# Performance work log

Measured on AMD Instinct MI355X. Metric: run time of the kernel, lower is better.

## Reference

```python
import jax, jax.numpy as jnp
import numpy as np

D_MODEL = 1024
NUM_LATENTS = 8
N_HEADS = 8
HEAD_DIM = D_MODEL // N_HEADS
LN_EPS = 1e-5
NEG_INF = -1e9


def setup_inputs() -> dict:
    key = jax.random.key(0)
    ks = jax.random.split(key, 9)
    B, S, d = 8, 8192, D_MODEL
    hidden_states = jax.random.normal(ks[0], (B, S, d), dtype=jnp.float32)
    attention_mask = jax.random.randint(ks[1], (B, S), 0, 2, dtype=jnp.int32)
    # guarantee at least one valid token per row
    attention_mask = attention_mask.at[:, 0].set(1)
    latent_queries = jax.random.normal(ks[2], (NUM_LATENTS, d), dtype=jnp.float32) * 0.02
    lim = 1.0 / np.sqrt(d)
    in_proj_weight = jax.random.uniform(ks[3], (3 * d, d), minval=-lim, maxval=lim, dtype=jnp.float32)
    in_proj_bias = jnp.zeros((3 * d,), jnp.float32)
    out_proj_weight = jax.random.uniform(ks[4], (d, d), minval=-lim, maxval=lim, dtype=jnp.float32)
    out_proj_bias = jnp.zeros((d,), jnp.float32)
    ln_gamma = jnp.ones((d,), jnp.float32)
    ln_beta = jnp.zeros((d,), jnp.float32)
    return {
        "hidden_states": hidden_states,
        "latent_queries": latent_queries,
        "in_proj_weight": in_proj_weight,
        "in_proj_bias": in_proj_bias,
        "out_proj_weight": out_proj_weight,
        "out_proj_bias": out_proj_bias,
        "ln_gamma": ln_gamma,
        "ln_beta": ln_beta,
        "attention_mask": attention_mask,
    }


def reference(hidden_states, latent_queries, in_proj_weight, in_proj_bias,
              out_proj_weight, out_proj_bias, ln_gamma, ln_beta, attention_mask):
    B, S, d = hidden_states.shape
    K, H, hd = NUM_LATENTS, N_HEADS, HEAD_DIM
    Wq, Wk, Wv = jnp.split(in_proj_weight, 3, axis=0)   # each [d, d]
    bq, bk, bv = jnp.split(in_proj_bias, 3, axis=0)
    # projections (queries shared over batch)
    q = latent_queries @ Wq.T + bq                      # [K, d]
    k = hidden_states @ Wk.T + bk                       # [B, S, d]
    v = hidden_states @ Wv.T + bv                       # [B, S, d]
    q = q.reshape(K, H, hd).transpose(1, 0, 2)          # [H, K, hd]
    k = k.reshape(B, S, H, hd).transpose(0, 2, 1, 3)    # [B, H, S, hd]
    v = v.reshape(B, S, H, hd).transpose(0, 2, 1, 3)    # [B, H, S, hd]
    scale = 1.0 / np.sqrt(hd)
    scores = jnp.einsum('hkd,bhsd->bhks', q, k) * scale  # [B, H, K, S]
    pad = (attention_mask == 0)[:, None, None, :]        # [B, 1, 1, S]
    scores = jnp.where(pad, NEG_INF, scores)
    attn = jax.nn.softmax(scores, axis=-1)
    ctx = jnp.einsum('bhks,bhsd->bhkd', attn, v)         # [B, H, K, hd]
    ctx = ctx.transpose(0, 2, 1, 3).reshape(B, K, d)     # [B, K, d]
    pooled = ctx @ out_proj_weight.T + out_proj_bias     # [B, K, d]
    # LayerNorm
    mu = pooled.mean(-1, keepdims=True)
    var = jnp.mean(jnp.square(pooled - mu), axis=-1, keepdims=True)
    pooled = (pooled - mu) * jax.lax.rsqrt(var + LN_EPS) * ln_gamma + ln_beta
    return pooled.mean(axis=1)                           # [B, d]
```

## Files before the change

kernel.cpp:

```cpp
#include <hip/hip_runtime.h>
#include <math.h>

#define D_M 1024
#define S_L 8192
#define B_N 8
#define H_N 8
#define HD_ 128
#define HK_ 64
#define SCALE_ 0.08838834764831845f
#define NEG_INF_ -1e9f
#define PITCH_ 40
#define AP_ 72

typedef _Float16 half8v __attribute__((ext_vector_type(8)));
typedef _Float16 half4v __attribute__((ext_vector_type(4)));
typedef float floatx4 __attribute__((ext_vector_type(4)));

__global__ void k_q(const float* __restrict__ lat, const float* __restrict__ W,
                    const float* __restrict__ bias, float* __restrict__ q) {
  int g = blockIdx.x * blockDim.x + threadIdx.x;
  int kidx = g >> 10, i = g & 1023;
  const float* wr = W + (size_t)i * D_M;
  const float* lr = lat + kidx * D_M;
  float acc = bias[i];
  #pragma unroll 4
  for (int t = 0; t < D_M; t += 4) {
    float4 w = *(const float4*)(wr + t);
    float4 l = *(const float4*)(lr + t);
    acc += w.x*l.x + w.y*l.y + w.z*l.z + w.w*l.w;
  }
  q[g] = acc;
}

__global__ void k_qt(const float* __restrict__ q, const float* __restrict__ W,
                     const float* __restrict__ bias, _Float16* __restrict__ qth,
                     float* __restrict__ qconst) {
  int g = blockIdx.x * blockDim.x + threadIdx.x;
  int hk = g >> 10, j = g & 1023;
  int h = hk >> 3, kidx = hk & 7;
  const float* qr = q + kidx * D_M + h * HD_;
  const float* wb = W + ((size_t)D_M + (size_t)h * HD_) * D_M + j;
  float acc = 0.f;
  #pragma unroll 4
  for (int dd = 0; dd < HD_; ++dd)
    acc += qr[dd] * wb[(size_t)dd * D_M];
  qth[g] = (_Float16)(acc * SCALE_);
  if (j == 0) {
    const float* bk = bias + D_M + h * HD_;
    float c = 0.f;
    for (int dd = 0; dd < HD_; ++dd) c += qr[dd] * bk[dd];
    qconst[hk] = c * SCALE_;
  }
}

__global__ __launch_bounds__(256) void k_scores3(
    const float* __restrict__ hsrc, const _Float16* __restrict__ qth,
    const float* __restrict__ qc, const int* __restrict__ mask,
    _Float16* __restrict__ ph, float* __restrict__ pm, float* __restrict__ pl) {
  __shared__ __align__(16) _Float16 As[128 * AP_];
  __shared__ __align__(16) _Float16 Bs[64 * AP_];
  __shared__ _Float16 pT[128][68];
  __shared__ int smask[128];
  __shared__ float qcs[64];
  const int tid = threadIdx.x;
  const int b = blockIdx.x >> 6;
  const int st = blockIdx.x & 63;
  const int s0 = st * 128;
  const int w = tid >> 6, l = tid & 63;
  const int row16 = l & 15, kc = l >> 4;
  if (tid < 128) smask[tid] = mask[b * S_L + s0 + tid];
  if (tid < 64) qcs[tid] = qc[tid];
  floatx4 acc[2][4];
  #pragma unroll
  for (int mf = 0; mf < 2; ++mf)
    #pragma unroll
    for (int nf = 0; nf < 4; ++nf) acc[mf][nf] = (floatx4){0.f, 0.f, 0.f, 0.f};

  const int r_ = tid >> 3, c_ = tid & 7;
  const float* hb = hsrc + ((size_t)b * S_L + s0) * D_M;
  float4 fa[4][2];
  half8v fb[2];
  #pragma unroll
  for (int p = 0; p < 4; ++p) {
    const float* pr = hb + (size_t)(p * 32 + r_) * D_M + c_ * 8;
    fa[p][0] = *(const float4*)pr; fa[p][1] = *(const float4*)(pr + 4);
  }
  fb[0] = *(const half8v*)(qth + (size_t)r_ * D_M + c_ * 8);
  fb[1] = *(const half8v*)(qth + (size_t)(r_ + 32) * D_M + c_ * 8);

  for (int k0 = 0; k0 < D_M; k0 += 64) {
    __syncthreads();
    #pragma unroll
    for (int p = 0; p < 4; ++p) {
      half8v hv;
      hv[0] = (_Float16)fa[p][0].x; hv[1] = (_Float16)fa[p][0].y;
      hv[2] = (_Float16)fa[p][0].z; hv[3] = (_Float16)fa[p][0].w;
      hv[4] = (_Float16)fa[p][1].x; hv[5] = (_Float16)fa[p][1].y;
      hv[6] = (_Float16)fa[p][1].z; hv[7] = (_Float16)fa[p][1].w;
      *(half8v*)&As[(p * 32 + r_) * AP_ + c_ * 8] = hv;
    }
    *(half8v*)&Bs[r_ * AP_ + c_ * 8] = fb[0];
    *(half8v*)&Bs[(r_ + 32) * AP_ + c_ * 8] = fb[1];
    if (k0 + 64 < D_M) {
      #pragma unroll
      for (int p = 0; p < 4; ++p) {
        const float* pr = hb + (size_t)(p * 32 + r_) * D_M + (k0 + 64) + c_ * 8;
        fa[p][0] = *(const float4*)pr; fa[p][1] = *(const float4*)(pr + 4);
      }
      fb[0] = *(const half8v*)(qth + (size_t)r_ * D_M + (k0 + 64) + c_ * 8);
      fb[1] = *(const half8v*)(qth + (size_t)(r_ + 32) * D_M + (k0 + 64) + c_ * 8);
    }
    __syncthreads();
    #pragma unroll
    for (int kk = 0; kk < 2; ++kk) {
      half8v af[2], bf4[4];
      #pragma unroll
      for (int mf = 0; mf < 2; ++mf)
        af[mf] = *(const half8v*)&As[(w * 32 + mf * 16 + row16) * AP_ + kk * 32 + kc * 8];
      #pragma unroll
      for (int nf = 0; nf < 4; ++nf)
        bf4[nf] = *(const half8v*)&Bs[(nf * 16 + row16) * AP_ + kk * 32 + kc * 8];
      #pragma unroll
      for (int mf = 0; mf < 2; ++mf)
        #pragma unroll
        for (int nf = 0; nf < 4; ++nf)
          acc[mf][nf] = __builtin_amdgcn_mfma_f32_16x16x32_f16(af[mf], bf4[nf], acc[mf][nf], 0, 0, 0);
    }
  }
  int msk[8];
  #pragma unroll
  for (int mf = 0; mf < 2; ++mf)
    #pragma unroll
    for (int r = 0; r < 4; ++r)
      msk[mf * 4 + r] = smask[w * 32 + mf * 16 + kc * 4 + r];
  #pragma unroll
  for (int nf = 0; nf < 4; ++nf) {
    int hk = nf * 16 + row16;
    float qcv = qcs[hk];
    float vals[8];
    float mloc = -3.4e38f;
    #pragma unroll
    for (int mf = 0; mf < 2; ++mf)
      #pragma unroll
      for (int r = 0; r < 4; ++r) {
        float v = msk[mf * 4 + r] ? (acc[mf][nf][r] + qcv) : NEG_INF_;
        vals[mf * 4 + r] = v;
        mloc = fmaxf(mloc, v);
      }
    mloc = fmaxf(mloc, __shfl_xor(mloc, 16, 64));
    mloc = fmaxf(mloc, __shfl_xor(mloc, 32, 64));
    float ls = 0.f;
    #pragma unroll
    for (int mf = 0; mf < 2; ++mf)
      #pragma unroll
      for (int r = 0; r < 4; ++r) {
        float e = __expf(vals[mf * 4 + r] - mloc);
        ls += e;
        pT[w * 32 + mf * 16 + kc * 4 + r][hk] = (_Float16)e;
      }
    ls += __shfl_xor(ls, 16, 64);
    ls += __shfl_xor(ls, 32, 64);
    if (kc == 0) {
      int idx = ((b * 64 + st) * 4 + w) * 64 + hk;
      pm[idx] = mloc;
      pl[idx] = ls;
    }
  }
  __syncthreads();
  {
    int hk2 = tid >> 2, q4 = tid & 3;
    _Float16* dst = ph + ((size_t)b * 64 + hk2) * S_L + s0 + q4 * 32;
    #pragma unroll
    for (int i = 0; i < 4; ++i) {
      half8v v;
      #pragma unroll
      for (int e = 0; e < 8; ++e) v[e] = pT[q4 * 32 + i * 8 + e][hk2];
      *(half8v*)(dst + i * 8) = v;
    }
  }
}

__global__ __launch_bounds__(256) void k_stats2b(
    const float* __restrict__ pm, const float* __restrict__ pl,
    float* __restrict__ lvinv, _Float16* __restrict__ ph) {
  __shared__ float red[256];
  int bh = blockIdx.x;
  int b = bh >> 6, hk = bh & 63;
  int tid = threadIdx.x;
  float m = pm[((size_t)b * 256 + tid) * 64 + hk];
  float lv = pl[((size_t)b * 256 + tid) * 64 + hk];
  red[tid] = m; __syncthreads();
  for (int off = 128; off > 0; off >>= 1) {
    if (tid < off) red[tid] = fmaxf(red[tid], red[tid + off]);
    __syncthreads();
  }
  float M = red[0]; __syncthreads();
  red[tid] = lv * __expf(m - M); __syncthreads();
  for (int off = 128; off > 0; off >>= 1) {
    if (tid < off) red[tid] += red[tid + off];
    __syncthreads();
  }
  if (tid == 0) lvinv[bh] = 1.f / red[0];
  float f = __expf(m - M);
  _Float16* pp = ph + (size_t)bh * S_L + tid * 32;
  #pragma unroll
  for (int i = 0; i < 4; ++i) {
    half8v v = *(half8v*)(pp + i * 8);
    #pragma unroll
    for (int e = 0; e < 8; ++e) v[e] = (_Float16)((float)v[e] * f);
    *(half8v*)(pp + i * 8) = v;
  }
}

__global__ __launch_bounds__(512) void k_part(
    const float* __restrict__ hsrc, const _Float16* __restrict__ ph,
    float* __restrict__ part) {
  __shared__ __align__(16) _Float16 htile[512 * PITCH_];
  const int tid = threadIdx.x;
  const int b  = blockIdx.x >> 5;
  const int jb = (blockIdx.x >> 4) & 1;
  const int sc = blockIdx.x & 15;
  const int w = tid >> 6, l = tid & 63;
  const int row16 = l & 15, kc = l >> 4;
  const int s_base = sc * 512;
  const float* hb = hsrc + (size_t)b * S_L * D_M + jb * 512;
  const _Float16* phb = ph + (size_t)b * HK_ * S_L;
  floatx4 acc[4][4];
  #pragma unroll
  for (int mf = 0; mf < 4; ++mf)
    #pragma unroll
    for (int nf = 0; nf < 4; ++nf) acc[mf][nf] = (floatx4){0.f, 0.f, 0.f, 0.f};

  const int jcol = tid;
  float colv[32];
  #pragma unroll
  for (int s = 0; s < 32; ++s)
    colv[s] = hb[(size_t)(s_base + s) * D_M + jcol];

  for (int t = 0; t < 16; ++t) {
    const int s0 = s_base + t * 32;
    __syncthreads();
    #pragma unroll
    for (int sb = 0; sb < 8; ++sb) {
      half4v hv;
      hv[0] = (_Float16)colv[sb * 4 + 0];
      hv[1] = (_Float16)colv[sb * 4 + 1];
      hv[2] = (_Float16)colv[sb * 4 + 2];
      hv[3] = (_Float16)colv[sb * 4 + 3];
      *(half4v*)&htile[jcol * PITCH_ + sb * 4] = hv;
    }
    __syncthreads();
    if (t < 15) {
      #pragma unroll
      for (int s = 0; s < 32; ++s)
        colv[s] = hb[(size_t)(s0 + 32 + s) * D_M + jcol];
    }
    half8v ap[4];
    #pragma unroll
    for (int mf = 0; mf < 4; ++mf)
      ap[mf] = *(const half8v*)(phb + (size_t)(mf * 16 + row16) * S_L + s0 + kc * 8);
    #pragma unroll
    for (int nf = 0; nf < 4; ++nf) {
      int j = w * 64 + nf * 16 + row16;
      half8v bv = *(const half8v*)&htile[j * PITCH_ + kc * 8];
      #pragma unroll
      for (int mf = 0; mf < 4; ++mf)
        acc[mf][nf] = __builtin_amdgcn_mfma_f32_16x16x32_f16(ap[mf], bv, acc[mf][nf], 0, 0, 0);
    }
  }
  #pragma unroll
  for (int mf = 0; mf < 4; ++mf)
    #pragma unroll
    for (int nf = 0; nf < 4; ++nf) {
      int j = w * 64 + nf * 16 + row16;
      #pragma unroll
      for (int r = 0; r < 4; ++r) {
        int hk = mf * 16 + kc * 4 + r;
        part[(((size_t)(b * 2 + jb) * 16 + sc) * HK_ + hk) * 512 + j] = acc[mf][nf][r];
      }
    }
}

__global__ void k_comb(const float* __restrict__ part, const float* __restrict__ lvinv,
                       float* __restrict__ ctxh) {
  int g = blockIdx.x * blockDim.x + threadIdx.x;
  int b = g >> 14;
  int rem = g & 16383;
  int hk = rem >> 8;
  int j4 = rem & 255;
  int jb = j4 >> 7;
  int jr4 = j4 & 127;
  const float* pb = part + ((size_t)(b * 2 + jb) * 16 * HK_ + hk) * 512 + jr4 * 4;
  float4 s = make_float4(0.f, 0.f, 0.f, 0.f);
  #pragma unroll
  for (int sc = 0; sc < 16; ++sc) {
    float4 v = *(const float4*)(pb + (size_t)sc * HK_ * 512);
    s.x += v.x; s.y += v.y; s.z += v.z; s.w += v.w;
  }
  float li = lvinv[b * 64 + hk];
  s.x *= li; s.y *= li; s.z *= li; s.w *= li;
  *(float4*)(ctxh + ((size_t)b * HK_ + hk) * D_M + j4 * 4) = s;
}

__global__ void k_ctx(const float* __restrict__ ctxh, const float* __restrict__ W,
                      const float* __restrict__ bias, float* __restrict__ ctx) {
  int g2 = blockIdx.x * blockDim.x + threadIdx.x;
  int o = g2 >> 2, kq = g2 & 3;
  int b = o >> 13, kidx = (o >> 10) & 7, i = o & 1023;
  int hk = (i >> 7) * 8 + kidx;
  const float* wr = W + ((size_t)2 * D_M + i) * D_M + kq * 256;
  const float* xr = ctxh + ((size_t)b * HK_ + hk) * D_M + kq * 256;
  float acc = 0.f;
  #pragma unroll 8
  for (int t = 0; t < 256; t += 4) {
    float4 w = *(const float4*)(wr + t);
    float4 x = *(const float4*)(xr + t);
    acc += w.x*x.x + w.y*x.y + w.z*x.z + w.w*x.w;
  }
  acc += __shfl_xor(acc, 1, 64);
  acc += __shfl_xor(acc, 2, 64);
  if (kq == 0) ctx[o] = acc + bias[2 * D_M + i];
}

__global__ void k_pool(const float* __restrict__ ctx, const float* __restrict__ W,
                       const float* __restrict__ bias, float* __restrict__ pooled) {
  int g2 = blockIdx.x * blockDim.x + threadIdx.x;
  int o = g2 >> 2, kq = g2 & 3;
  int b = o >> 13, kidx = (o >> 10) & 7, i = o & 1023;
  const float* wr = W + (size_t)i * D_M + kq * 256;
  const float* xr = ctx + ((size_t)b * 8 + kidx) * D_M + kq * 256;
  float acc = 0.f;
  #pragma unroll 8
  for (int t = 0; t < 256; t += 4) {
    float4 w = *(const float4*)(wr + t);
    float4 x = *(const float4*)(xr + t);
    acc += w.x*x.x + w.y*x.y + w.z*x.z + w.w*x.w;
  }
  acc += __shfl_xor(acc, 1, 64);
  acc += __shfl_xor(acc, 2, 64);
  if (kq == 0) pooled[o] = acc + bias[i];
}

__global__ void k_ln(const float* __restrict__ pooled, const float* __restrict__ gamma,
                     const float* __restrict__ beta, float* __restrict__ out) {
  __shared__ float red[256];
  int b = blockIdx.x, tid = threadIdx.x;
  float acc[4] = {0.f, 0.f, 0.f, 0.f};
  for (int kidx = 0; kidx < 8; ++kidx) {
    const float* row = pooled + ((size_t)b * 8 + kidx) * D_M;
    float v[4]; float s = 0.f;
    #pragma unroll
    for (int c = 0; c < 4; ++c) { v[c] = row[tid + 256 * c]; s += v[c]; }
    red[tid] = s; __syncthreads();
    for (int off = 128; off > 0; off >>= 1) {
      if (tid < off) red[tid] += red[tid + off];
      __syncthreads();
    }
    float mu = red[0] * (1.f / 1024.f);
    __syncthreads();
    float ss = 0.f;
    #pragma unroll
    for (int c = 0; c < 4; ++c) { float dd = v[c] - mu; ss += dd * dd; }
    red[tid] = ss; __syncthreads();
    for (int off = 128; off > 0; off >>= 1) {
      if (tid < off) red[tid] += red[tid + off];
      __syncthreads();
    }
    float rstd = rsqrtf(red[0] * (1.f / 1024.f) + 1e-5f);
    __syncthreads();
    #pragma unroll
    for (int c = 0; c < 4; ++c) {
      int i = tid + 256 * c;
      acc[c] += ((v[c] - mu) * rstd * gamma[i] + beta[i]) * 0.125f;
    }
  }
  #pragma unroll
  for (int c = 0; c < 4; ++c) out[(size_t)b * D_M + tid + 256 * c] = acc[c];
}

extern "C" void kernel_launch(void* const* d_in, const int* in_sizes, int n_in,
                              void* d_out, int out_size, void* d_ws, size_t ws_size,
                              hipStream_t stream) {
  const float* hidden = (const float*)d_in[0];
  const float* latent = (const float*)d_in[1];
  const float* w_in   = (const float*)d_in[2];
  const float* b_in   = (const float*)d_in[3];
  const float* w_out  = (const float*)d_in[4];
  const float* b_out  = (const float*)d_in[5];
  const float* gamma  = (const float*)d_in[6];
  const float* beta   = (const float*)d_in[7];
  const int*   mask   = (const int*)d_in[8];
  float* out = (float*)d_out;
  float* ws = (float*)d_ws;
  float* q      = ws;
  float* qc     = q + 8192;
  float* lvinv  = qc + 64;
  float* pm     = lvinv + 512;
  float* pl     = pm + 131072;
  _Float16* qth = (_Float16*)(pl + 131072);
  _Float16* ph  = (_Float16*)(pl + 131072 + 32768);
  float* part   = pl + 131072 + 32768 + 2097152;
  float* ctxh   = part + 8388608;
  float* ctx    = ctxh + 524288;
  float* pooled = ctx + 65536;

  k_q       <<<32,   256, 0, stream>>>(latent, w_in, b_in, q);
  k_qt      <<<256,  256, 0, stream>>>(q, w_in, b_in, qth, qc);
  k_scores3 <<<512,  256, 0, stream>>>(hidden, qth, qc, mask, ph, pm, pl);
  k_stats2b <<<512,  256, 0, stream>>>(pm, pl, lvinv, ph);
  k_part    <<<256,  512, 0, stream>>>(hidden, ph, part);
  k_comb    <<<512,  256, 0, stream>>>(part, lvinv, ctxh);
  k_ctx     <<<1024, 256, 0, stream>>>(ctxh, w_in, b_in, ctx);
  k_pool    <<<1024, 256, 0, stream>>>(ctx, w_out, b_out, pooled);
  k_ln      <<<8,    256, 0, stream>>>(pooled, gamma, beta, out);
}
```

Before: 315.3 us.

## Defer softmax rescale into k_part and double thread parallelism in scores/part kernels

k_scores3 now runs 512 threads per block, each wave owning 16 rows instead of 32, and reuses the As buffer for the transposed probability tile to cut LDS. The stats kernel no longer rewrites the fp16 probability buffer. It emits per-tile scale factors instead, which k_part applies while loading the probabilities, removing a full read-modify-write pass over ph. k_part splits the column dimension into four blocks of 256, giving 512 blocks with fewer accumulators each. The cost is more sync overhead per unit of work, extra scale loads and multiplies in k_part, and re-reading the probability rows across four column blocks.

```diff
diff --git a/kernel.cpp b/kernel.cpp
--- a/kernel.cpp
+++ b/kernel.cpp
@@ -53,13 +53,12 @@
   }
 }
 
-__global__ __launch_bounds__(256) void k_scores3(
+__global__ __launch_bounds__(512, 2) void k_scores3(
     const float* __restrict__ hsrc, const _Float16* __restrict__ qth,
     const float* __restrict__ qc, const int* __restrict__ mask,
     _Float16* __restrict__ ph, float* __restrict__ pm, float* __restrict__ pl) {
   __shared__ __align__(16) _Float16 As[128 * AP_];
   __shared__ __align__(16) _Float16 Bs[64 * AP_];
-  __shared__ _Float16 pT[128][68];
   __shared__ int smask[128];
   __shared__ float qcs[64];
   const int tid = threadIdx.x;
@@ -70,198 +69,181 @@
   const int row16 = l & 15, kc = l >> 4;
   if (tid < 128) smask[tid] = mask[b * S_L + s0 + tid];
   if (tid < 64) qcs[tid] = qc[tid];
-  floatx4 acc[2][4];
-  #pragma unroll
-  for (int mf = 0; mf < 2; ++mf)
-    #pragma unroll
-    for (int nf = 0; nf < 4; ++nf) acc[mf][nf] = (floatx4){0.f, 0.f, 0.f, 0.f};
+  floatx4 acc[4];
+  #pragma unroll
+  for (int nf = 0; nf < 4; ++nf) acc[nf] = (floatx4){0.f, 0.f, 0.f, 0.f};
 
   const int r_ = tid >> 3, c_ = tid & 7;
   const float* hb = hsrc + ((size_t)b * S_L + s0) * D_M;
-  float4 fa[4][2];
-  half8v fb[2];
-  #pragma unroll
-  for (int p = 0; p < 4; ++p) {
-    const float* pr = hb + (size_t)(p * 32 + r_) * D_M + c_ * 8;
+  float4 fa[2][2];
+  half8v fb;
+  #pragma unroll
+  for (int p = 0; p < 2; ++p) {
+    const float* pr = hb + (size_t)(p * 64 + r_) * D_M + c_ * 8;
     fa[p][0] = *(const float4*)pr; fa[p][1] = *(const float4*)(pr + 4);
   }
-  fb[0] = *(const half8v*)(qth + (size_t)r_ * D_M + c_ * 8);
-  fb[1] = *(const half8v*)(qth + (size_t)(r_ + 32) * D_M + c_ * 8);
+  fb = *(const half8v*)(qth + (size_t)r_ * D_M + c_ * 8);
 
   for (int k0 = 0; k0 < D_M; k0 += 64) {
     __syncthreads();
     #pragma unroll
-    for (int p = 0; p < 4; ++p) {
+    for (int p = 0; p < 2; ++p) {
       half8v hv;
       hv[0] = (_Float16)fa[p][0].x; hv[1] = (_Float16)fa[p][0].y;
       hv[2] = (_Float16)fa[p][0].z; hv[3] = (_Float16)fa[p][0].w;
       hv[4] = (_Float16)fa[p][1].x; hv[5] = (_Float16)fa[p][1].y;
       hv[6] = (_Float16)fa[p][1].z; hv[7] = (_Float16)fa[p][1].w;
-      *(half8v*)&As[(p * 32 + r_) * AP_ + c_ * 8] = hv;
-    }
-    *(half8v*)&Bs[r_ * AP_ + c_ * 8] = fb[0];
-    *(half8v*)&Bs[(r_ + 32) * AP_ + c_ * 8] = fb[1];
+      *(half8v*)&As[(p * 64 + r_) * AP_ + c_ * 8] = hv;
+    }
+    *(half8v*)&Bs[r_ * AP_ + c_ * 8] = fb;
     if (k0 + 64 < D_M) {
       #pragma unroll
-      for (int p = 0; p < 4; ++p) {
-        const float* pr = hb + (size_t)(p * 32 + r_) * D_M + (k0 + 64) + c_ * 8;
+      for (int p = 0; p < 2; ++p) {
+        const float* pr = hb + (size_t)(p * 64 + r_) * D_M + (k0 + 64) + c_ * 8;
         fa[p][0] = *(const float4*)pr; fa[p][1] = *(const float4*)(pr + 4);
       }
-      fb[0] = *(const half8v*)(qth + (size_t)r_ * D_M + (k0 + 64) + c_ * 8);
-      fb[1] = *(const half8v*)(qth + (size_t)(r_ + 32) * D_M + (k0 + 64) + c_ * 8);
+      fb = *(const half8v*)(qth + (size_t)r_ * D_M + (k0 + 64) + c_ * 8);
     }
     __syncthreads();
     #pragma unroll
     for (int kk = 0; kk < 2; ++kk) {
-      half8v af[2], bf4[4];
-      #pragma unroll
-      for (int mf = 0; mf < 2; ++mf)
-        af[mf] = *(const half8v*)&As[(w * 32 + mf * 16 + row16) * AP_ + kk * 32 + kc * 8];
-      #pragma unroll
-      for (int nf = 0; nf < 4; ++nf)
-        bf4[nf] = *(const half8v*)&Bs[(nf * 16 + row16) * AP_ + kk * 32 + kc * 8];
-      #pragma unroll
-      for (int mf = 0; mf < 2; ++mf)
-        #pragma unroll
-        for (int nf = 0; nf < 4; ++nf)
-          acc[mf][nf] = __builtin_amdgcn_mfma_f32_16x16x32_f16(af[mf], bf4[nf], acc[mf][nf], 0, 0, 0);
-    }
-  }
-  int msk[8];
-  #pragma unroll
-  for (int mf = 0; mf < 2; ++mf)
-    #pragma unroll
-    for (int r = 0; r < 4; ++r)
-      msk[mf * 4 + r] = smask[w * 32 + mf * 16 + kc * 4 + r];
+      half8v af = *(const half8v*)&As[(w * 16 + row16) * AP_ + kk * 32 + kc * 8];
+      #pragma unroll
+      for (int nf = 0; nf < 4; ++nf) {
+        half8v bf = *(const half8v*)&Bs[(nf * 16 + row16) * AP_ + kk * 32 + kc * 8];
+        acc[nf] = __builtin_amdgcn_mfma_f32_16x16x32_f16(af, bf, acc[nf], 0, 0, 0);
+      }
+    }
+  }
+  __syncthreads();
+  _Float16 (*pT)[68] = (_Float16 (*)[68])As;
+  int msk[4];
+  #pragma unroll
+  for (int r = 0; r < 4; ++r) msk[r] = smask[w * 16 + kc * 4 + r];
   #pragma unroll
   for (int nf = 0; nf < 4; ++nf) {
     int hk = nf * 16 + row16;
     float qcv = qcs[hk];
-    float vals[8];
+    float vals[4];
     float mloc = -3.4e38f;
     #pragma unroll
-    for (int mf = 0; mf < 2; ++mf)
-      #pragma unroll
-      for (int r = 0; r < 4; ++r) {
-        float v = msk[mf * 4 + r] ? (acc[mf][nf][r] + qcv) : NEG_INF_;
-        vals[mf * 4 + r] = v;
-        mloc = fmaxf(mloc, v);
-      }
+    for (int r = 0; r < 4; ++r) {
+      float v = msk[r] ? (acc[nf][r] + qcv) : NEG_INF_;
+      vals[r] = v;
+      mloc = fmaxf(mloc, v);
+    }
     mloc = fmaxf(mloc, __shfl_xor(mloc, 16, 64));
     mloc = fmaxf(mloc, __shfl_xor(mloc, 32, 64));
     float ls = 0.f;
     #pragma unroll
-    for (int mf = 0; mf < 2; ++mf)
-      #pragma unroll
-      for (int r = 0; r < 4; ++r) {
-        float e = __expf(vals[mf * 4 + r] - mloc);
-        ls += e;
-        pT[w * 32 + mf * 16 + kc * 4 + r][hk] = (_Float16)e;
-      }
+    for (int r = 0; r < 4; ++r) {
+      float e = __expf(vals[r] - mloc);
+      ls += e;
+      pT[w * 16 + kc * 4 + r][hk] = (_Float16)e;
+    }
     ls += __shfl_xor(ls, 16, 64);
     ls += __shfl_xor(ls, 32, 64);
     if (kc == 0) {
-      int idx = ((b * 64 + st) * 4 + w) * 64 + hk;
+      int idx = ((b * 64 + st) * 8 + w) * 64 + hk;
       pm[idx] = mloc;
       pl[idx] = ls;
     }
   }
   __syncthreads();
   {
-    int hk2 = tid >> 2, q4 = tid & 3;
-    _Float16* dst = ph + ((size_t)b * 64 + hk2) * S_L + s0 + q4 * 32;
-    #pragma unroll
-    for (int i = 0; i < 4; ++i) {
+    int hk2 = tid >> 3, q8 = tid & 7;
+    _Float16* dst = ph + ((size_t)b * 64 + hk2) * S_L + s0 + q8 * 16;
+    #pragma unroll
+    for (int i = 0; i < 2; ++i) {
       half8v v;
       #pragma unroll
-      for (int e = 0; e < 8; ++e) v[e] = pT[q4 * 32 + i * 8 + e][hk2];
+      for (int e = 0; e < 8; ++e) v[e] = pT[q8 * 16 + i * 8 + e][hk2];
       *(half8v*)(dst + i * 8) = v;
     }
   }
 }
 
-__global__ __launch_bounds__(256) void k_stats2b(
+__global__ __launch_bounds__(512) void k_stats2c(
     const float* __restrict__ pm, const float* __restrict__ pl,
-    float* __restrict__ lvinv, _Float16* __restrict__ ph) {
-  __shared__ float red[256];
+    float* __restrict__ lvinv, float* __restrict__ sf) {
+  __shared__ float red[512];
   int bh = blockIdx.x;
   int b = bh >> 6, hk = bh & 63;
   int tid = threadIdx.x;
-  float m = pm[((size_t)b * 256 + tid) * 64 + hk];
-  float lv = pl[((size_t)b * 256 + tid) * 64 + hk];
+  float m = pm[((size_t)b * 512 + tid) * 64 + hk];
+  float lv = pl[((size_t)b * 512 + tid) * 64 + hk];
   red[tid] = m; __syncthreads();
-  for (int off = 128; off > 0; off >>= 1) {
+  for (int off = 256; off > 0; off >>= 1) {
     if (tid < off) red[tid] = fmaxf(red[tid], red[tid + off]);
     __syncthreads();
   }
   float M = red[0]; __syncthreads();
-  red[tid] = lv * __expf(m - M); __syncthreads();
-  for (int off = 128; off > 0; off >>= 1) {
+  float f = __expf(m - M);
+  red[tid] = lv * f; __syncthreads();
+  for (int off = 256; off > 0; off >>= 1) {
     if (tid < off) red[tid] += red[tid + off];
     __syncthreads();
   }
   if (tid == 0) lvinv[bh] = 1.f / red[0];
-  float f = __expf(m - M);
-  _Float16* pp = ph + (size_t)bh * S_L + tid * 32;
-  #pragma unroll
-  for (int i = 0; i < 4; ++i) {
-    half8v v = *(half8v*)(pp + i * 8);
-    #pragma unroll
-    for (int e = 0; e < 8; ++e) v[e] = (_Float16)((float)v[e] * f);
-    *(half8v*)(pp + i * 8) = v;
-  }
-}
-
-__global__ __launch_bounds__(512) void k_part(
+  sf[(size_t)bh * 512 + tid] = f;
+}
+
+__global__ __launch_bounds__(512, 2) void k_part(
     const float* __restrict__ hsrc, const _Float16* __restrict__ ph,
-    float* __restrict__ part) {
-  __shared__ __align__(16) _Float16 htile[512 * PITCH_];
+    const float* __restrict__ sf, float* __restrict__ part) {
+  __shared__ __align__(16) _Float16 htile[256 * PITCH_];
   const int tid = threadIdx.x;
-  const int b  = blockIdx.x >> 5;
-  const int jb = (blockIdx.x >> 4) & 1;
+  const int b  = blockIdx.x >> 6;
+  const int jb = (blockIdx.x >> 4) & 3;
   const int sc = blockIdx.x & 15;
   const int w = tid >> 6, l = tid & 63;
   const int row16 = l & 15, kc = l >> 4;
   const int s_base = sc * 512;
-  const float* hb = hsrc + (size_t)b * S_L * D_M + jb * 512;
+  const float* hb = hsrc + (size_t)b * S_L * D_M + jb * 256;
   const _Float16* phb = ph + (size_t)b * HK_ * S_L;
-  floatx4 acc[4][4];
+  const float* sfb = sf + (size_t)b * HK_ * 512;
+  floatx4 acc[4][2];
   #pragma unroll
   for (int mf = 0; mf < 4; ++mf)
     #pragma unroll
-    for (int nf = 0; nf < 4; ++nf) acc[mf][nf] = (floatx4){0.f, 0.f, 0.f, 0.f};
-
-  const int jcol = tid;
-  float colv[32];
-  #pragma unroll
-  for (int s = 0; s < 32; ++s)
-    colv[s] = hb[(size_t)(s_base + s) * D_M + jcol];
+    for (int nf = 0; nf < 2; ++nf) acc[mf][nf] = (floatx4){0.f, 0.f, 0.f, 0.f};
+
+  const int jc = tid & 255, shh = tid >> 8;
+  float colv[16];
+  #pragma unroll
+  for (int i = 0; i < 16; ++i)
+    colv[i] = hb[(size_t)(s_base + shh * 16 + i) * D_M + jc];
 
   for (int t = 0; t < 16; ++t) {
     const int s0 = s_base + t * 32;
     __syncthreads();
     #pragma unroll
-    for (int sb = 0; sb < 8; ++sb) {
+    for (int i4 = 0; i4 < 4; ++i4) {
       half4v hv;
-      hv[0] = (_Float16)colv[sb * 4 + 0];
-      hv[1] = (_Float16)colv[sb * 4 + 1];
-      hv[2] = (_Float16)colv[sb * 4 + 2];
-      hv[3] = (_Float16)colv[sb * 4 + 3];
-      *(half4v*)&htile[jcol * PITCH_ + sb * 4] = hv;
+      hv[0] = (_Float16)colv[i4 * 4 + 0];
+      hv[1] = (_Float16)colv[i4 * 4 + 1];
+      hv[2] = (_Float16)colv[i4 * 4 + 2];
+      hv[3] = (_Float16)colv[i4 * 4 + 3];
+      *(half4v*)&htile[jc * PITCH_ + shh * 16 + i4 * 4] = hv;
     }
     __syncthreads();
     if (t < 15) {
       #pragma unroll
-      for (int s = 0; s < 32; ++s)
-        colv[s] = hb[(size_t)(s0 + 32 + s) * D_M + jcol];
-    }
+      for (int i = 0; i < 16; ++i)
+        colv[i] = hb[(size_t)(s0 + 32 + shh * 16 + i) * D_M + jc];
+    }
+    const int tile = sc * 32 + t * 2 + (kc >> 1);
     half8v ap[4];
     #pragma unroll
-    for (int mf = 0; mf < 4; ++mf)
-      ap[mf] = *(const half8v*)(phb + (size_t)(mf * 16 + row16) * S_L + s0 + kc * 8);
-    #pragma unroll
-    for (int nf = 0; nf < 4; ++nf) {
-      int j = w * 64 + nf * 16 + row16;
+    for (int mf = 0; mf < 4; ++mf) {
+      half8v raw = *(const half8v*)(phb + (size_t)(mf * 16 + row16) * S_L + s0 + kc * 8);
+      _Float16 s16 = (_Float16)sfb[(size_t)(mf * 16 + row16) * 512 + tile];
+      #pragma unroll
+      for (int e = 0; e < 8; ++e) ap[mf][e] = raw[e] * s16;
+    }
+    #pragma unroll
+    for (int nf = 0; nf < 2; ++nf) {
+      int j = w * 32 + nf * 16 + row16;
       half8v bv = *(const half8v*)&htile[j * PITCH_ + kc * 8];
       #pragma unroll
       for (int mf = 0; mf < 4; ++mf)
@@ -271,12 +253,12 @@
   #pragma unroll
   for (int mf = 0; mf < 4; ++mf)
     #pragma unroll
-    for (int nf = 0; nf < 4; ++nf) {
-      int j = w * 64 + nf * 16 + row16;
+    for (int nf = 0; nf < 2; ++nf) {
+      int j = w * 32 + nf * 16 + row16;
       #pragma unroll
       for (int r = 0; r < 4; ++r) {
         int hk = mf * 16 + kc * 4 + r;
-        part[(((size_t)(b * 2 + jb) * 16 + sc) * HK_ + hk) * 512 + j] = acc[mf][nf][r];
+        part[(((size_t)(b * 4 + jb) * 16 + sc) * HK_ + hk) * 256 + j] = acc[mf][nf][r];
       }
     }
 }
@@ -288,13 +270,13 @@
   int rem = g & 16383;
   int hk = rem >> 8;
   int j4 = rem & 255;
-  int jb = j4 >> 7;
-  int jr4 = j4 & 127;
-  const float* pb = part + ((size_t)(b * 2 + jb) * 16 * HK_ + hk) * 512 + jr4 * 4;
+  int jb = j4 >> 6;
+  int jr4 = j4 & 63;
+  const float* pb = part + ((size_t)(b * 4 + jb) * 16 * HK_ + hk) * 256 + jr4 * 4;
   float4 s = make_float4(0.f, 0.f, 0.f, 0.f);
   #pragma unroll
   for (int sc = 0; sc < 16; ++sc) {
-    float4 v = *(const float4*)(pb + (size_t)sc * HK_ * 512);
+    float4 v = *(const float4*)(pb + (size_t)sc * HK_ * 256);
     s.x += v.x; s.y += v.y; s.z += v.z; s.w += v.w;
   }
   float li = lvinv[b * 64 + hk];
@@ -396,19 +378,20 @@
   float* qc     = q + 8192;
   float* lvinv  = qc + 64;
   float* pm     = lvinv + 512;
-  float* pl     = pm + 131072;
-  _Float16* qth = (_Float16*)(pl + 131072);
-  _Float16* ph  = (_Float16*)(pl + 131072 + 32768);
-  float* part   = pl + 131072 + 32768 + 2097152;
+  float* pl     = pm + 262144;
+  float* sf     = pl + 262144;
+  _Float16* qth = (_Float16*)(sf + 262144);
+  _Float16* ph  = (_Float16*)(sf + 262144 + 32768);
+  float* part   = sf + 262144 + 32768 + 2097152;
   float* ctxh   = part + 8388608;
   float* ctx    = ctxh + 524288;
   float* pooled = ctx + 65536;
 
   k_q       <<<32,   256, 0, stream>>>(latent, w_in, b_in, q);
   k_qt      <<<256,  256, 0, stream>>>(q, w_in, b_in, qth, qc);
-  k_scores3 <<<512,  256, 0, stream>>>(hidden, qth, qc, mask, ph, pm, pl);
-  k_stats2b <<<512,  256, 0, stream>>>(pm, pl, lvinv, ph);
-  k_part    <<<256,  512, 0, stream>>>(hidden, ph, part);
+  k_scores3 <<<512,  512, 0, stream>>>(hidden, qth, qc, mask, ph, pm, pl);
+  k_stats2c <<<512,  512, 0, stream>>>(pm, pl, lvinv, sf);
+  k_part    <<<512,  512, 0, stream>>>(hidden, ph, sf, part);
   k_comb    <<<512,  256, 0, stream>>>(part, lvinv, ctxh);
   k_ctx     <<<1024, 256, 0, stream>>>(ctxh, w_in, b_in, ctx);
   k_pool    <<<1024, 256, 0, stream>>>(ctx, w_out, b_out, pooled);
```

Result: slower. 350.3 us (+11.1%).

## Defer softmax rescale into k_part and alias score transpose buffer in LDS

Applied to the files above, without the earlier changes.

The stats kernel no longer rewrites the whole fp16 probability buffer with per-tile exp(m-M) factors. It stores the per-tile factors to a small array, and k_part multiplies each loaded probability fragment by its factor before the MFMA. This removes a full read-modify-write pass over ph (8M fp16). Separately, k_scores3 reuses the As LDS tile for the transpose buffer after a barrier and requests 4 blocks per CU via launch bounds, which raises occupancy but may constrain registers.

```diff
diff --git a/kernel.cpp b/kernel.cpp
--- a/kernel.cpp
+++ b/kernel.cpp
@@ -53,13 +53,12 @@
   }
 }
 
-__global__ __launch_bounds__(256) void k_scores3(
+__global__ __launch_bounds__(256, 4) void k_scores3(
     const float* __restrict__ hsrc, const _Float16* __restrict__ qth,
     const float* __restrict__ qc, const int* __restrict__ mask,
     _Float16* __restrict__ ph, float* __restrict__ pm, float* __restrict__ pl) {
   __shared__ __align__(16) _Float16 As[128 * AP_];
   __shared__ __align__(16) _Float16 Bs[64 * AP_];
-  __shared__ _Float16 pT[128][68];
   __shared__ int smask[128];
   __shared__ float qcs[64];
   const int tid = threadIdx.x;
@@ -127,6 +126,8 @@
           acc[mf][nf] = __builtin_amdgcn_mfma_f32_16x16x32_f16(af[mf], bf4[nf], acc[mf][nf], 0, 0, 0);
     }
   }
+  __syncthreads();
+  _Float16 (*pT)[68] = (_Float16 (*)[68])As;
   int msk[8];
   #pragma unroll
   for (int mf = 0; mf < 2; ++mf)
@@ -180,9 +181,9 @@
   }
 }
 
-__global__ __launch_bounds__(256) void k_stats2b(
+__global__ __launch_bounds__(256) void k_stats2c(
     const float* __restrict__ pm, const float* __restrict__ pl,
-    float* __restrict__ lvinv, _Float16* __restrict__ ph) {
+    float* __restrict__ lvinv, float* __restrict__ sf) {
   __shared__ float red[256];
   int bh = blockIdx.x;
   int b = bh >> 6, hk = bh & 63;
@@ -195,26 +196,19 @@
     __syncthreads();
   }
   float M = red[0]; __syncthreads();
-  red[tid] = lv * __expf(m - M); __syncthreads();
+  float f = __expf(m - M);
+  red[tid] = lv * f; __syncthreads();
   for (int off = 128; off > 0; off >>= 1) {
     if (tid < off) red[tid] += red[tid + off];
     __syncthreads();
   }
   if (tid == 0) lvinv[bh] = 1.f / red[0];
-  float f = __expf(m - M);
-  _Float16* pp = ph + (size_t)bh * S_L + tid * 32;
-  #pragma unroll
-  for (int i = 0; i < 4; ++i) {
-    half8v v = *(half8v*)(pp + i * 8);
-    #pragma unroll
-    for (int e = 0; e < 8; ++e) v[e] = (_Float16)((float)v[e] * f);
-    *(half8v*)(pp + i * 8) = v;
-  }
+  sf[(size_t)bh * 256 + tid] = f;
 }
 
 __global__ __launch_bounds__(512) void k_part(
     const float* __restrict__ hsrc, const _Float16* __restrict__ ph,
-    float* __restrict__ part) {
+    const float* __restrict__ sf, float* __restrict__ part) {
   __shared__ __align__(16) _Float16 htile[512 * PITCH_];
   const int tid = threadIdx.x;
   const int b  = blockIdx.x >> 5;
@@ -225,6 +219,7 @@
   const int s_base = sc * 512;
   const float* hb = hsrc + (size_t)b * S_L * D_M + jb * 512;
   const _Float16* phb = ph + (size_t)b * HK_ * S_L;
+  const float* sfb = sf + (size_t)b * HK_ * 256;
   floatx4 acc[4][4];
   #pragma unroll
   for (int mf = 0; mf < 4; ++mf)
@@ -255,10 +250,15 @@
       for (int s = 0; s < 32; ++s)
         colv[s] = hb[(size_t)(s0 + 32 + s) * D_M + jcol];
     }
+    const int t32 = sc * 16 + t;
     half8v ap[4];
     #pragma unroll
-    for (int mf = 0; mf < 4; ++mf)
-      ap[mf] = *(const half8v*)(phb + (size_t)(mf * 16 + row16) * S_L + s0 + kc * 8);
+    for (int mf = 0; mf < 4; ++mf) {
+      half8v raw = *(const half8v*)(phb + (size_t)(mf * 16 + row16) * S_L + s0 + kc * 8);
+      _Float16 fv = (_Float16)sfb[(size_t)(mf * 16 + row16) * 256 + t32];
+      #pragma unroll
+      for (int e = 0; e < 8; ++e) ap[mf][e] = raw[e] * fv;
+    }
     #pragma unroll
     for (int nf = 0; nf < 4; ++nf) {
       int j = w * 64 + nf * 16 + row16;
@@ -397,9 +397,10 @@
   float* lvinv  = qc + 64;
   float* pm     = lvinv + 512;
   float* pl     = pm + 131072;
-  _Float16* qth = (_Float16*)(pl + 131072);
-  _Float16* ph  = (_Float16*)(pl + 131072 + 32768);
-  float* part   = pl + 131072 + 32768 + 2097152;
+  float* sf     = pl + 131072;
+  _Float16* qth = (_Float16*)(sf + 131072);
+  _Float16* ph  = (_Float16*)(sf + 131072 + 32768);
+  float* part   = sf + 131072 + 32768 + 2097152;
   float* ctxh   = part + 8388608;
   float* ctx    = ctxh + 524288;
   float* pooled = ctx + 65536;
@@ -407,8 +408,8 @@
   k_q       <<<32,   256, 0, stream>>>(latent, w_in, b_in, q);
   k_qt      <<<256,  256, 0, stream>>>(q, w_in, b_in, qth, qc);
   k_scores3 <<<512,  256, 0, stream>>>(hidden, qth, qc, mask, ph, pm, pl);
-  k_stats2b <<<512,  256, 0, stream>>>(pm, pl, lvinv, ph);
-  k_part    <<<256,  512, 0, stream>>>(hidden, ph, part);
+  k_stats2c <<<512,  256, 0, stream>>>(pm, pl, lvinv, sf);
+  k_part    <<<256,  512, 0, stream>>>(hidden, ph, sf, part);
   k_comb    <<<512,  256, 0, stream>>>(part, lvinv, ctxh);
   k_ctx     <<<1024, 256, 0, stream>>>(ctxh, w_in, b_in, ctx);
   k_pool    <<<1024, 256, 0, stream>>>(ctx, w_out, b_out, pooled);
```

After: 323.3 us. +2.5%, slower.

## Compact valid tokens and skip masked-out sequence tiles

Applied to the files above, without the earlier changes.

Adds a count kernel and a gather kernel that pack each batch's unmasked token rows into a contiguous workspace buffer. The scores, stats, partial-context and combine kernels then read the packed buffer and return early for tiles past the rounded-up valid count, replacing the per-token mask lookup with an index-versus-count test. The aim is to skip MFMA and softmax work on padded tokens, at the cost of an extra read and write pass over the valid rows. The pad rows up to the next multiple of 512 are never written and come from uninitialised workspace, so garbage values there could reach the probability-times-value products.

```diff
diff --git a/kernel.cpp b/kernel.cpp
--- a/kernel.cpp
+++ b/kernel.cpp
@@ -53,22 +53,78 @@
   }
 }
 
+__global__ __launch_bounds__(512) void k_cnt(const int* __restrict__ mask,
+                                             int* __restrict__ cbase,
+                                             int* __restrict__ cnt) {
+  __shared__ int wcnt[8];
+  __shared__ int ccnt[64];
+  int b = blockIdx.x, tid = threadIdx.x, w = tid >> 6, lane = tid & 63;
+  int vs[16];
+  #pragma unroll
+  for (int it = 0; it < 16; ++it) vs[it] = mask[b * S_L + it * 512 + tid];
+  for (int it = 0; it < 16; ++it) {
+    unsigned long long m = __ballot(vs[it] != 0);
+    if (lane == 0) wcnt[w] = __popcll(m);
+    __syncthreads();
+    if (tid < 4) ccnt[it * 4 + tid] = wcnt[2 * tid] + wcnt[2 * tid + 1];
+    __syncthreads();
+  }
+  if (tid == 0) {
+    int base = 0;
+    for (int c = 0; c < 64; ++c) { cbase[b * 64 + c] = base; base += ccnt[c]; }
+    cnt[b] = base;
+  }
+}
+
+__global__ __launch_bounds__(128) void k_gather(const float* __restrict__ hidden,
+                                                const int* __restrict__ mask,
+                                                const int* __restrict__ cbase,
+                                                float* __restrict__ hcomp) {
+  __shared__ int slot_of[128];
+  __shared__ int wcnt[2];
+  __shared__ int woff[3];
+  int blk = blockIdx.x;
+  int b = blk >> 6, c = blk & 63;
+  int tid = threadIdx.x, w = tid >> 6, lane = tid & 63;
+  int valid = mask[b * S_L + c * 128 + tid] != 0;
+  unsigned long long m = __ballot(valid);
+  int rank = __popcll(m & ((1ull << lane) - 1ull));
+  if (lane == 0) wcnt[w] = __popcll(m);
+  __syncthreads();
+  if (tid == 0) { woff[0] = 0; woff[1] = wcnt[0]; woff[2] = wcnt[0] + wcnt[1]; }
+  __syncthreads();
+  if (valid) slot_of[woff[w] + rank] = tid;
+  __syncthreads();
+  int nv = woff[2];
+  int base = cbase[b * 64 + c];
+  for (int v = w; v < nv; v += 2) {
+    const float* src = hidden + ((size_t)b * S_L + c * 128 + slot_of[v]) * D_M;
+    float* dst = hcomp + ((size_t)b * S_L + base + v) * D_M;
+    #pragma unroll
+    for (int q4 = 0; q4 < 4; ++q4) {
+      float4 val = *(const float4*)(src + q4 * 256 + lane * 4);
+      *(float4*)(dst + q4 * 256 + lane * 4) = val;
+    }
+  }
+}
+
 __global__ __launch_bounds__(256) void k_scores3(
-    const float* __restrict__ hsrc, const _Float16* __restrict__ qth,
-    const float* __restrict__ qc, const int* __restrict__ mask,
+    const float* __restrict__ hcomp, const _Float16* __restrict__ qth,
+    const float* __restrict__ qc, const int* __restrict__ cnt,
     _Float16* __restrict__ ph, float* __restrict__ pm, float* __restrict__ pl) {
   __shared__ __align__(16) _Float16 As[128 * AP_];
   __shared__ __align__(16) _Float16 Bs[64 * AP_];
   __shared__ _Float16 pT[128][68];
-  __shared__ int smask[128];
   __shared__ float qcs[64];
   const int tid = threadIdx.x;
   const int b = blockIdx.x >> 6;
   const int st = blockIdx.x & 63;
   const int s0 = st * 128;
+  const int cb = cnt[b];
+  const int SPb = ((cb + 511) >> 9) << 9;
+  if (s0 >= SPb) return;
   const int w = tid >> 6, l = tid & 63;
   const int row16 = l & 15, kc = l >> 4;
-  if (tid < 128) smask[tid] = mask[b * S_L + s0 + tid];
   if (tid < 64) qcs[tid] = qc[tid];
   floatx4 acc[2][4];
   #pragma unroll
@@ -77,7 +133,7 @@
     for (int nf = 0; nf < 4; ++nf) acc[mf][nf] = (floatx4){0.f, 0.f, 0.f, 0.f};
 
   const int r_ = tid >> 3, c_ = tid & 7;
-  const float* hb = hsrc + ((size_t)b * S_L + s0) * D_M;
+  const float* hb = hcomp + ((size_t)b * S_L + s0) * D_M;
   float4 fa[4][2];
   half8v fb[2];
   #pragma unroll
@@ -132,7 +188,7 @@
   for (int mf = 0; mf < 2; ++mf)
     #pragma unroll
     for (int r = 0; r < 4; ++r)
-      msk[mf * 4 + r] = smask[w * 32 + mf * 16 + kc * 4 + r];
+      msk[mf * 4 + r] = (s0 + w * 32 + mf * 16 + kc * 4 + r) < cb;
   #pragma unroll
   for (int nf = 0; nf < 4; ++nf) {
     int hk = nf * 16 + row16;
@@ -182,13 +238,18 @@
 
 __global__ __launch_bounds__(256) void k_stats2b(
     const float* __restrict__ pm, const float* __restrict__ pl,
-    float* __restrict__ lvinv, _Float16* __restrict__ ph) {
+    const int* __restrict__ cnt, float* __restrict__ lvinv, _Float16* __restrict__ ph) {
   __shared__ float red[256];
   int bh = blockIdx.x;
   int b = bh >> 6, hk = bh & 63;
   int tid = threadIdx.x;
-  float m = pm[((size_t)b * 256 + tid) * 64 + hk];
-  float lv = pl[((size_t)b * 256 + tid) * 64 + hk];
+  const int cb = cnt[b];
+  const int ntile = (((cb + 511) >> 9) << 9) >> 5;
+  float m = -3.4e38f, lv = 0.f;
+  if (tid < ntile) {
+    m = pm[((size_t)b * 256 + tid) * 64 + hk];
+    lv = pl[((size_t)b * 256 + tid) * 64 + hk];
+  }
   red[tid] = m; __syncthreads();
   for (int off = 128; off > 0; off >>= 1) {
     if (tid < off) red[tid] = fmaxf(red[tid], red[tid + off]);
@@ -201,29 +262,33 @@
     __syncthreads();
   }
   if (tid == 0) lvinv[bh] = 1.f / red[0];
-  float f = __expf(m - M);
-  _Float16* pp = ph + (size_t)bh * S_L + tid * 32;
-  #pragma unroll
-  for (int i = 0; i < 4; ++i) {
-    half8v v = *(half8v*)(pp + i * 8);
-    #pragma unroll
-    for (int e = 0; e < 8; ++e) v[e] = (_Float16)((float)v[e] * f);
-    *(half8v*)(pp + i * 8) = v;
+  if (tid < ntile) {
+    float f = __expf(m - M);
+    _Float16* pp = ph + (size_t)bh * S_L + tid * 32;
+    #pragma unroll
+    for (int i = 0; i < 4; ++i) {
+      half8v v = *(half8v*)(pp + i * 8);
+      #pragma unroll
+      for (int e = 0; e < 8; ++e) v[e] = (_Float16)((float)v[e] * f);
+      *(half8v*)(pp + i * 8) = v;
+    }
   }
 }
 
 __global__ __launch_bounds__(512) void k_part(
-    const float* __restrict__ hsrc, const _Float16* __restrict__ ph,
-    float* __restrict__ part) {
+    const float* __restrict__ hcomp, const _Float16* __restrict__ ph,
+    const int* __restrict__ cnt, float* __restrict__ part) {
   __shared__ __align__(16) _Float16 htile[512 * PITCH_];
   const int tid = threadIdx.x;
   const int b  = blockIdx.x >> 5;
   const int jb = (blockIdx.x >> 4) & 1;
   const int sc = blockIdx.x & 15;
+  const int SPb = ((cnt[b] + 511) >> 9) << 9;
+  if (sc * 512 >= SPb) return;
   const int w = tid >> 6, l = tid & 63;
   const int row16 = l & 15, kc = l >> 4;
   const int s_base = sc * 512;
-  const float* hb = hsrc + (size_t)b * S_L * D_M + jb * 512;
+  const float* hb = hcomp + (size_t)b * S_L * D_M + jb * 512;
   const _Float16* phb = ph + (size_t)b * HK_ * S_L;
   floatx4 acc[4][4];
   #pragma unroll
@@ -282,7 +347,7 @@
 }
 
 __global__ void k_comb(const float* __restrict__ part, const float* __restrict__ lvinv,
-                       float* __restrict__ ctxh) {
+                       const int* __restrict__ cnt, float* __restrict__ ctxh) {
   int g = blockIdx.x * blockDim.x + threadIdx.x;
   int b = g >> 14;
   int rem = g & 16383;
@@ -290,10 +355,10 @@
   int j4 = rem & 255;
   int jb = j4 >> 7;
   int jr4 = j4 & 127;
+  const int nsc = (((cnt[b] + 511) >> 9) << 9) >> 9;
   const float* pb = part + ((size_t)(b * 2 + jb) * 16 * HK_ + hk) * 512 + jr4 * 4;
   float4 s = make_float4(0.f, 0.f, 0.f, 0.f);
-  #pragma unroll
-  for (int sc = 0; sc < 16; ++sc) {
+  for (int sc = 0; sc < nsc; ++sc) {
     float4 v = *(const float4*)(pb + (size_t)sc * HK_ * 512);
     s.x += v.x; s.y += v.y; s.z += v.z; s.w += v.w;
   }
@@ -403,13 +468,18 @@
   float* ctxh   = part + 8388608;
   float* ctx    = ctxh + 524288;
   float* pooled = ctx + 65536;
+  int*   cnt    = (int*)(pooled + 65536);
+  int*   cbase  = (int*)(pooled + 65536 + 16);
+  float* hcomp  = pooled + 65536 + 16 + 512;
 
   k_q       <<<32,   256, 0, stream>>>(latent, w_in, b_in, q);
   k_qt      <<<256,  256, 0, stream>>>(q, w_in, b_in, qth, qc);
-  k_scores3 <<<512,  256, 0, stream>>>(hidden, qth, qc, mask, ph, pm, pl);
-  k_stats2b <<<512,  256, 0, stream>>>(pm, pl, lvinv, ph);
-  k_part    <<<256,  512, 0, stream>>>(hidden, ph, part);
-  k_comb    <<<512,  256, 0, stream>>>(part, lvinv, ctxh);
+  k_cnt     <<<8,    512, 0, stream>>>(mask, cbase, cnt);
+  k_gather  <<<512,  128, 0, stream>>>(hidden, mask, cbase, hcomp);
+  k_scores3 <<<512,  256, 0, stream>>>(hcomp, qth, qc, cnt, ph, pm, pl);
+  k_stats2b <<<512,  256, 0, stream>>>(pm, pl, cnt, lvinv, ph);
+  k_part    <<<256,  512, 0, stream>>>(hcomp, ph, cnt, part);
+  k_comb    <<<512,  256, 0, stream>>>(part, lvinv, cnt, ctxh);
   k_ctx     <<<1024, 256, 0, stream>>>(ctxh, w_in, b_in, ctx);
   k_pool    <<<1024, 256, 0, stream>>>(ctx, w_out, b_out, pooled);
   k_ln      <<<8,    256, 0, stream>>>(pooled, gamma, beta, out);
```

After: 351.0 us. 1.11x slower.
